# Optimization experiments

Hardware: AMD Instinct MI355X
Metric: run time of the kernel (lower is better)

Reference implementation:

```python
import jax, jax.numpy as jnp
import numpy as np

B, N, D, H, E, K = 8, 1024, 768, 12, 4, 9
PAD = (K - 1) // 2


def _ln(x, g, b, eps=1e-5):
    m = jnp.mean(x, -1, keepdims=True)
    v = jnp.var(x, -1, keepdims=True)
    return (x - m) * jax.lax.rsqrt(v + eps) * g + b


def setup_inputs() -> dict:
    key = jax.random.key(0)
    ks = jax.random.split(key, 12)
    w = lambda k, s: jax.random.normal(k, s, jnp.float32) * 0.02
    return {
        "x": jax.random.normal(ks[0], (B, N, D), jnp.float32),
        "ff1_ln_g": jnp.ones(D), "ff1_ln_b": jnp.zeros(D),
        "ff1_w1": w(ks[1], (D, E * D)), "ff1_b1": jnp.zeros(E * D),
        "ff1_w2": w(ks[2], (E * D, D)), "ff1_b2": jnp.zeros(D),
        "attn_ln_g": jnp.ones(D), "attn_ln_b": jnp.zeros(D),
        "qkv_w": w(ks[3], (D, 3 * D)), "qkv_b": jnp.zeros(3 * D),
        "proj_w": w(ks[4], (D, D)), "proj_b": jnp.zeros(D),
        "rel_table": w(ks[5], (2 * N - 1, H)),
        "conv_ln_g": jnp.ones(D), "conv_ln_b": jnp.zeros(D),
        "pwin_w": w(ks[6], (2 * D, D)), "pwin_b": jnp.zeros(2 * D),
        "dw_w": w(ks[7], (D, 1, K)), "dw_b": jnp.zeros(D),
        "bn_g": jnp.ones(D), "bn_b": jnp.zeros(D),
        "pwout_w": w(ks[8], (D, D)), "pwout_b": jnp.zeros(D),
        "ff2_ln_g": jnp.ones(D), "ff2_ln_b": jnp.zeros(D),
        "ff2_w1": w(ks[9], (D, E * D)), "ff2_b1": jnp.zeros(E * D),
        "ff2_w2": w(ks[10], (E * D, D)), "ff2_b2": jnp.zeros(D),
        "fin_ln_g": jnp.ones(D), "fin_ln_b": jnp.zeros(D),
    }


def _ffn(x, g, b, w1, b1, w2, b2):
    h = jax.nn.gelu(_ln(x, g, b) @ w1 + b1, approximate=False)
    return h @ w2 + b2


def _attn(x, qkv_w, qkv_b, proj_w, proj_b, rel_table):
    b_, n_, c = x.shape
    hd = c // H
    qkv = (x @ qkv_w + qkv_b).reshape(b_, n_, 3, H, hd).transpose(2, 0, 3, 1, 4)
    q, k, v = qkv[0], qkv[1], qkv[2]  # (B, H, N, hd)
    scores = jnp.einsum('bhqd,bhkd->bhqk', q, k) * (hd ** -0.5)
    coords = jnp.arange(n_)
    idx = coords[None, :] - coords[:, None] + N - 1  # (N, N) in [0, 2N-2]
    bias = rel_table[idx].transpose(2, 0, 1)  # (H, N, N)
    a = jax.nn.softmax(scores + bias[None], axis=-1)
    out = jnp.einsum('bhqk,bhkd->bhqd', a, v).transpose(0, 2, 1, 3).reshape(b_, n_, c)
    return out @ proj_w + proj_b


def _conv(x, g, b, pwin_w, pwin_b, dw_w, dw_b, bn_g, bn_b, pwout_w, pwout_b):
    y = _ln(x, g, b) @ pwin_w.T + pwin_b  # pointwise-in conv as matmul -> (B, N, 2D)
    u, gate = jnp.split(y, 2, axis=-1)
    y = (u * jax.nn.sigmoid(gate)).transpose(0, 2, 1)  # GLU over channels -> (B, D, N)
    y = jax.lax.conv_general_dilated(
        y, dw_w, (1,), [(PAD, PAD)], feature_group_count=D,
        dimension_numbers=('NCH', 'OIH', 'NCH')) + dw_b[None, :, None]
    m = jnp.mean(y, (0, 2), keepdims=True)  # BatchNorm1d, training-mode batch stats
    v = jnp.var(y, (0, 2), keepdims=True)
    y = (y - m) * jax.lax.rsqrt(v + 1e-5) * bn_g[None, :, None] + bn_b[None, :, None]
    y = y * jax.nn.sigmoid(y)  # SiLU
    y = jnp.einsum('bcn,oc->bno', y, pwout_w) + pwout_b  # pointwise-out, back to (B, N, D)
    return y


def reference(x, ff1_ln_g, ff1_ln_b, ff1_w1, ff1_b1, ff1_w2, ff1_b2,
              attn_ln_g, attn_ln_b, qkv_w, qkv_b, proj_w, proj_b, rel_table,
              conv_ln_g, conv_ln_b, pwin_w, pwin_b, dw_w, dw_b, bn_g, bn_b,
              pwout_w, pwout_b, ff2_ln_g, ff2_ln_b, ff2_w1, ff2_b1, ff2_w2, ff2_b2,
              fin_ln_g, fin_ln_b):
    x = x + 0.5 * _ffn(x, ff1_ln_g, ff1_ln_b, ff1_w1, ff1_b1, ff1_w2, ff1_b2)
    x = x + _attn(_ln(x, attn_ln_g, attn_ln_b), qkv_w, qkv_b, proj_w, proj_b, rel_table)
    x = x + _conv(x, conv_ln_g, conv_ln_b, pwin_w, pwin_b, dw_w, dw_b, bn_g, bn_b, pwout_w, pwout_b)
    x = x + 0.5 * _ffn(x, ff2_ln_g, ff2_ln_b, ff2_w1, ff2_b1, ff2_w2, ff2_b2)
    return _ln(x, fin_ln_g, fin_ln_b)
```

## Files before the change

### kernel.cpp

```cpp
#include <hip/hip_runtime.h>
#include <math.h>

#define Bb 8
#define Nn 1024
#define Dd 768
#define Hh 12
#define Mm 8192

typedef __attribute__((ext_vector_type(4))) float f32x4;
typedef __attribute__((ext_vector_type(8))) __bf16 bf16x8;

__device__ __forceinline__ float bf2f(unsigned short u) {
  union { unsigned int i; float f; } v; v.i = ((unsigned int)u) << 16; return v.f;
}
__device__ __forceinline__ unsigned short f2bf(float f) {
  union { float f; unsigned int i; } v; v.f = f;
  unsigned int u = v.i;
  return (unsigned short)((u + 0x7FFFu + ((u >> 16) & 1u)) >> 16);
}
__device__ __forceinline__ unsigned int pack2bf(float a, float b) {
  union { __bf16 h[2]; unsigned int u; } x;
  x.h[0] = (__bf16)a; x.h[1] = (__bf16)b; return x.u;
}

__device__ __forceinline__ void gload16(const void* g, void* l) {
  __builtin_amdgcn_global_load_lds(
      (const __attribute__((address_space(1))) unsigned int*)g,
      (__attribute__((address_space(3))) unsigned int*)l, 16, 0, 0);
}

__device__ __forceinline__ float gelu_f(float v) {
  const float z = fabsf(v) * 0.7071067811865475f;
  const float t = __builtin_amdgcn_rcpf(1.f + 0.3275911f * z);
  const float poly = t*(0.254829592f + t*(-0.284496736f + t*(1.421413741f +
                     t*(-1.453152027f + t*1.061405429f))));
  float er = 1.f - poly * __expf(-z * z);
  er = copysignf(er, v);
  return 0.5f * v * (1.f + er);
}

template<int EPI, int NT>
__global__ __launch_bounds__(256)
void gemm_bt(const unsigned short* __restrict__ A,
             const unsigned short* __restrict__ Bt,
             const float* __restrict__ bias,
             unsigned short* __restrict__ Cbf,
             float* __restrict__ Res,
             int M, int N, int K, float scale)
{
  __shared__ __align__(16) unsigned short Asm[128*32];
  __shared__ __align__(16) unsigned short Bsm[NT*32];
  const int tid = threadIdx.x;
  const int wv = tid >> 6, lane = tid & 63;
  const int lr = lane & 15, lg = lane >> 4;
  const int wr = wv >> 1, wc = wv & 1;
  constexpr int JN = NT / 32;

  const int gx = gridDim.x, gy = gridDim.y;
  const int nwg = gx * gy;
  const int lin = blockIdx.y * gx + blockIdx.x;
  const int q8 = nwg >> 3, r8 = nwg & 7;
  const int xcd = lin & 7, lidx = lin >> 3;
  const int wg = ((xcd < r8) ? xcd * (q8 + 1) : r8 * (q8 + 1) + (xcd - r8) * q8) + lidx;
  const int bx = wg % gx;
  const int by = wg / gx;

  const int n0 = bx * NT, m0 = by * 128;

  f32x4 acc[4][JN] = {};

  const int schk = (lane & 3) * 8;
  const unsigned short* Ag = A + (size_t)(m0 + wv*32 + (lane >> 2))*K + schk;
  unsigned short* Al = Asm + wv*1024;
  const unsigned short* Bg;
  unsigned short* Bl;
  if (NT == 128) { Bg = Bt + (size_t)(n0 + wv*32 + (lane >> 2))*K + schk; Bl = Bsm + wv*1024; }
  else           { Bg = Bt + (size_t)(n0 + wv*16 + (lane >> 2))*K + schk; Bl = Bsm + wv*512; }
  const size_t rstep = (size_t)16 * K;

  for (int kt = 0; kt < K; kt += 32) {
    gload16(Ag + kt,          Al);
    gload16(Ag + kt + rstep,  Al + 512);
    gload16(Bg + kt,          Bl);
    if (NT == 128) gload16(Bg + kt + rstep, Bl + 512);
    __syncthreads();
    bf16x8 af[4], bfr[JN];
#pragma unroll
    for (int i = 0; i < 4; i++) af[i]  = *(const bf16x8*)&Asm[(wr*64 + i*16 + lr)*32 + lg*8];
#pragma unroll
    for (int j = 0; j < JN; j++) bfr[j] = *(const bf16x8*)&Bsm[(wc*(NT/2) + j*16 + lr)*32 + lg*8];
#pragma unroll
    for (int i = 0; i < 4; i++)
#pragma unroll
      for (int j = 0; j < JN; j++)
        acc[i][j] = __builtin_amdgcn_mfma_f32_16x16x32_bf16(af[i], bfr[j], acc[i][j], 0, 0, 0);
    __syncthreads();
  }

#pragma unroll
  for (int i = 0; i < 4; i++) {
    const int rg = m0 + wr*64 + i*16 + lg*4;
    if (EPI == 3) {
#pragma unroll
      for (int j = 0; j < JN; j += 2) {
        const int cgu = n0 + wc*(NT/2) + j*16 + lr;
        const float bu = bias[cgu], bg = bias[cgu + 16];
        const int ocol = (n0 >> 1) + wc*(NT/4) + (j >> 1)*16 + lr;
#pragma unroll
        for (int e = 0; e < 4; e++) {
          float u  = acc[i][j][e]   + bu;
          float gt = acc[i][j+1][e] + bg;
          Cbf[(size_t)(rg + e) * (N >> 1) + ocol] = f2bf(u / (1.f + __expf(-gt)));
        }
      }
    } else {
#pragma unroll
      for (int j = 0; j < JN; j++) {
        const int cg = n0 + wc*(NT/2) + j*16 + lr;
        const float bv = bias[cg];
#pragma unroll
        for (int e = 0; e < 4; e++) {
          float v = acc[i][j][e] + bv;
          const size_t idx = (size_t)(rg + e) * N + cg;
          if (EPI == 1) {
            Cbf[idx] = f2bf(gelu_f(v));
          } else if (EPI == 0) {
            Cbf[idx] = f2bf(v);
          } else {
            Res[idx] += scale * v;
          }
        }
      }
    }
  }
}

template<bool OBF>
__global__ __launch_bounds__(256)
void ln_kernel(const float* x, const float* __restrict__ g,
               const float* __restrict__ b, void* out)
{
  const int row = blockIdx.x, tid = threadIdx.x;
  const float* xr = x + (size_t)row * Dd;
  float v0 = xr[tid], v1 = xr[tid+256], v2 = xr[tid+512];
  float s = v0+v1+v2, q = v0*v0+v1*v1+v2*v2;
  for (int off = 32; off; off >>= 1) { s += __shfl_down(s, off); q += __shfl_down(q, off); }
  __shared__ float ps[4], pq[4];
  if ((tid & 63) == 0) { ps[tid>>6] = s; pq[tid>>6] = q; }
  __syncthreads();
  s = ps[0]+ps[1]+ps[2]+ps[3]; q = pq[0]+pq[1]+pq[2]+pq[3];
  const float mean = s * (1.f/768.f);
  const float rstd = rsqrtf(q*(1.f/768.f) - mean*mean + 1e-5f);
  float y0 = (v0-mean)*rstd*g[tid]     + b[tid];
  float y1 = (v1-mean)*rstd*g[tid+256] + b[tid+256];
  float y2 = (v2-mean)*rstd*g[tid+512] + b[tid+512];
  if (OBF) {
    unsigned short* o = (unsigned short*)out + (size_t)row * Dd;
    o[tid] = f2bf(y0); o[tid+256] = f2bf(y1); o[tid+512] = f2bf(y2);
  } else {
    float* o = (float*)out + (size_t)row * Dd;
    o[tid] = y0; o[tid+256] = y1; o[tid+512] = y2;
  }
}

__global__ __launch_bounds__(256)
void transpose_w(const float* __restrict__ src, unsigned short* __restrict__ dst,
                 int K, int N)
{
  __shared__ float t[32][33];
  const int tx = threadIdx.x, ty = threadIdx.y;
  const int n0 = blockIdx.x * 32, k0 = blockIdx.y * 32;
#pragma unroll
  for (int i = 0; i < 4; i++) t[ty + i*8][tx] = src[(size_t)(k0 + ty + i*8)*N + n0 + tx];
  __syncthreads();
#pragma unroll
  for (int i = 0; i < 4; i++)
    dst[(size_t)(n0 + ty + i*8)*K + k0 + tx] = f2bf(t[tx][ty + i*8]);
}

__global__ __launch_bounds__(256)
void convert_bf(const float* __restrict__ src, unsigned short* __restrict__ dst, int n)
{
  for (int i = blockIdx.x*256 + threadIdx.x; i < n; i += gridDim.x*256)
    dst[i] = f2bf(src[i]);
}

__global__ __launch_bounds__(256)
void perm_pwin(const float* __restrict__ w, const float* __restrict__ b,
               unsigned short* __restrict__ wt, float* __restrict__ bperm)
{
  const int r = blockIdx.x;
  const int blk = r >> 7, g = (r >> 4) & 7, t = r & 15;
  const int orig = blk*64 + ((g >> 1) << 4) + t + ((g & 1) ? 768 : 0);
  const float* src = w + (size_t)orig * 768;
  unsigned short* dst = wt + (size_t)r * 768;
  const int tid = threadIdx.x;
  dst[tid] = f2bf(src[tid]); dst[tid+256] = f2bf(src[tid+256]); dst[tid+512] = f2bf(src[tid+512]);
  if (tid == 0) bperm[r] = b[orig];
}

__global__ __launch_bounds__(256)
void dw_tr(const float* __restrict__ src, float* __restrict__ dst)
{
  const int id = blockIdx.x*256 + threadIdx.x;
  if (id >= 9*768) return;
  const int k = id / 768, d = id % 768;
  dst[id] = src[d*9 + k];
}

__global__ __launch_bounds__(256)
void v_transpose(const unsigned short* __restrict__ big, unsigned short* __restrict__ vtr)
{
  __shared__ unsigned short t[64][72];
  const int bh = blockIdx.x;
  const int b = bh / Hh, h = bh % Hh;
  const int n0 = blockIdx.y * 64;
  const int tid = threadIdx.x;
  const int r = tid >> 2, cc = (tid & 3) * 16;
  const size_t gb = (size_t)(b*Nn + n0 + r)*2304 + 1536 + h*64 + cc;
  *(bf16x8*)&t[r][cc]     = *(const bf16x8*)(big + gb);
  *(bf16x8*)&t[r][cc + 8] = *(const bf16x8*)(big + gb + 8);
  __syncthreads();
  const int d = tid >> 2, nn = (tid & 3) * 16;
  bf16x8 o0, o1;
#pragma unroll
  for (int i = 0; i < 8; i++) o0[i] = *(const __bf16*)&t[nn + i][d];
#pragma unroll
  for (int i = 0; i < 8; i++) o1[i] = *(const __bf16*)&t[nn + 8 + i][d];
  unsigned short* dst = vtr + ((size_t)bh*64 + d)*Nn + n0 + nn;
  *(bf16x8*)dst = o0;
  *(bf16x8*)(dst + 8) = o1;
}

__global__ __launch_bounds__(256)
void attn_kernel(const unsigned short* __restrict__ qkv,
                 const unsigned short* __restrict__ vtr,
                 const float* __restrict__ rel,
                 unsigned short* __restrict__ out)
{
  const int bh = blockIdx.x; const int b = bh / Hh, h = bh % Hh;
  const int q0 = blockIdx.y * 64;
  const int tid = threadIdx.x, wv = tid >> 6, lane = tid & 63;
  const int lr = lane & 15, lg = lane >> 4;

  __shared__ __align__(16) unsigned short Kl[64*72];
  __shared__ __align__(16) unsigned short Vt[64*72 + 64];
  __shared__ __align__(16) unsigned short Pl[4*16*72];
  __shared__ float relh[2048];

  for (int i = tid; i < 2047; i += 256) relh[i] = rel[(size_t)i*Hh + h];

  const size_t qrow = (size_t)(b*Nn + q0 + wv*16 + lr);
  const bf16x8 qf0 = *(const bf16x8*)(qkv + qrow*2304 + h*64 + lg*8);
  const bf16x8 qf1 = *(const bf16x8*)(qkv + qrow*2304 + h*64 + 32 + lg*8);

  const int sd = tid >> 2;
  const int sc = (tid & 3) * 16;
  unsigned short* Pw = Pl + wv*16*72;

  f32x4 O[4] = {};
  float mrow = -1e30f, lsum = 0.f;
  const int qq = q0 + wv*16 + lr;

  __syncthreads();

  for (int kt = 0; kt < Nn; kt += 64) {
    {
      const size_t gk = (size_t)(b*Nn + kt + sd)*2304 + 768 + h*64 + sc;
      *(bf16x8*)&Kl[sd*72 + sc]     = *(const bf16x8*)(qkv + gk);
      *(bf16x8*)&Kl[sd*72 + sc + 8] = *(const bf16x8*)(qkv + gk + 8);
      const size_t gv = ((size_t)bh*64 + sd)*Nn + kt + sc;
      const int vb = sd*72 + (sd>>4)*16 + sc;
      *(bf16x8*)&Vt[vb]     = *(const bf16x8*)(vtr + gv);
      *(bf16x8*)&Vt[vb + 8] = *(const bf16x8*)(vtr + gv + 8);
    }
    __syncthreads();

    f32x4 s[4] = {};
#pragma unroll
    for (int kb = 0; kb < 4; kb++) {
      bf16x8 kfa = *(const bf16x8*)&Kl[(kb*16 + lr)*72 + lg*8];
      bf16x8 kfb = *(const bf16x8*)&Kl[(kb*16 + lr)*72 + 32 + lg*8];
      s[kb] = __builtin_amdgcn_mfma_f32_16x16x32_bf16(kfa, qf0, s[kb], 0, 0, 0);
      s[kb] = __builtin_amdgcn_mfma_f32_16x16x32_bf16(kfb, qf1, s[kb], 0, 0, 0);
    }

    const int bidx = kt - qq + (Nn - 1);
    float v[4][4]; float r = -1e30f;
#pragma unroll
    for (int kb = 0; kb < 4; kb++)
#pragma unroll
      for (int j = 0; j < 4; j++) {
        float t = s[kb][j]*0.125f + relh[bidx + kb*16 + lg*4 + j];
        v[kb][j] = t; r = fmaxf(r, t);
      }
    r = fmaxf(r, __shfl_xor(r, 16)); r = fmaxf(r, __shfl_xor(r, 32));

    if (!__all(r <= mrow + 8.f)) {
      const float mn = fmaxf(mrow, r);
      const float al = __expf(mrow - mn);
      mrow = mn;
      lsum *= al;
#pragma unroll
      for (int ni = 0; ni < 4; ni++) {
        O[ni][0]*=al; O[ni][1]*=al; O[ni][2]*=al; O[ni][3]*=al;
      }
    }

    float rs = 0.f;
    unsigned int pk[8];
#pragma unroll
    for (int kb = 0; kb < 4; kb++) {
      float p0 = __expf(v[kb][0]-mrow), p1 = __expf(v[kb][1]-mrow);
      float p2 = __expf(v[kb][2]-mrow), p3 = __expf(v[kb][3]-mrow);
      rs += (p0+p1) + (p2+p3);
      pk[kb*2]   = pack2bf(p0, p1);
      pk[kb*2+1] = pack2bf(p2, p3);
    }
    rs += __shfl_xor(rs, 16); rs += __shfl_xor(rs, 32);
    lsum += rs;

#pragma unroll
    for (int kb0 = 0; kb0 < 4; kb0++) {
      const int kb = (kb0 + lg) & 3;
      *(unsigned int*)&Pw[lr*72 + kb*16 + lg*4]     = pk[kb*2];
      *(unsigned int*)&Pw[lr*72 + kb*16 + lg*4 + 2] = pk[kb*2+1];
    }

    bf16x8 pf0 = *(const bf16x8*)&Pw[lr*72 + lg*8];
    bf16x8 pf1 = *(const bf16x8*)&Pw[lr*72 + 32 + lg*8];
#pragma unroll
    for (int dt = 0; dt < 4; dt++) {
      bf16x8 vf0 = *(const bf16x8*)&Vt[(dt*16 + lr)*72 + dt*16 + lg*8];
      bf16x8 vf1 = *(const bf16x8*)&Vt[(dt*16 + lr)*72 + dt*16 + 32 + lg*8];
      O[dt] = __builtin_amdgcn_mfma_f32_16x16x32_bf16(vf0, pf0, O[dt], 0, 0, 0);
      O[dt] = __builtin_amdgcn_mfma_f32_16x16x32_bf16(vf1, pf1, O[dt], 0, 0, 0);
    }
    __syncthreads();
  }

  const float rl = 1.f / lsum;
#pragma unroll
  for (int dt = 0; dt < 4; dt++) {
    ushort4 o4;
    o4.x = f2bf(O[dt][0]*rl); o4.y = f2bf(O[dt][1]*rl);
    o4.z = f2bf(O[dt][2]*rl); o4.w = f2bf(O[dt][3]*rl);
    *(ushort4*)(out + (size_t)(b*Nn + qq)*Dd + h*64 + dt*16 + lg*4) = o4;
  }
}

__global__ __launch_bounds__(256)
void dwconv(const unsigned short* __restrict__ glu, const float* __restrict__ dwwT,
            const float* __restrict__ dwb, unsigned short* __restrict__ z)
{
  const int id = blockIdx.x*256 + threadIdx.x;
  if (id >= Mm*96) return;
  const int row = id / 96, c8 = (id % 96) * 8;
  const int n = row % Nn;
  float acc[8] = {};
#pragma unroll
  for (int k = 0; k < 9; k++) {
    const int nn = n + k - 4;
    if (nn >= 0 && nn < Nn) {
      bf16x8 gv = *(const bf16x8*)&glu[(size_t)(row + k - 4)*768 + c8];
      const float4 w0 = *(const float4*)&dwwT[k*768 + c8];
      const float4 w1 = *(const float4*)&dwwT[k*768 + c8 + 4];
      acc[0] += w0.x*(float)gv[0]; acc[1] += w0.y*(float)gv[1];
      acc[2] += w0.z*(float)gv[2]; acc[3] += w0.w*(float)gv[3];
      acc[4] += w1.x*(float)gv[4]; acc[5] += w1.y*(float)gv[5];
      acc[6] += w1.z*(float)gv[6]; acc[7] += w1.w*(float)gv[7];
    }
  }
  bf16x8 o;
#pragma unroll
  for (int e = 0; e < 8; e++) o[e] = (__bf16)(acc[e] + dwb[c8+e]);
  *(bf16x8*)&z[(size_t)row*768 + c8] = o;
}

__global__ __launch_bounds__(256)
void bn_part(const unsigned short* __restrict__ z, float* __restrict__ psum,
             float* __restrict__ psq)
{
  const int blk = blockIdx.x, tid = threadIdx.x;
  float s[3] = {0,0,0}, q[3] = {0,0,0};
  for (int r = 0; r < 128; r++) {
    const unsigned short* row = z + (size_t)(blk*128 + r) * Dd;
#pragma unroll
    for (int i = 0; i < 3; i++) { float v = bf2f(row[tid + i*256]); s[i] += v; q[i] += v*v; }
  }
#pragma unroll
  for (int i = 0; i < 3; i++) {
    psum[(size_t)blk*Dd + tid + i*256] = s[i];
    psq [(size_t)blk*Dd + tid + i*256] = q[i];
  }
}

__global__ __launch_bounds__(256)
void bn_final(const float* __restrict__ psum, const float* __restrict__ psq,
              const float* __restrict__ g, const float* __restrict__ bb,
              float* __restrict__ scale, float* __restrict__ shift)
{
  const int c = blockIdx.x*256 + threadIdx.x;
  if (c >= Dd) return;
  float s = 0.f, q = 0.f;
  for (int i = 0; i < 64; i++) { s += psum[(size_t)i*Dd + c]; q += psq[(size_t)i*Dd + c]; }
  const float mean = s / (float)Mm;
  const float var  = q / (float)Mm - mean*mean;
  const float sc = g[c] * rsqrtf(var + 1e-5f);
  scale[c] = sc; shift[c] = bb[c] - mean*sc;
}

__global__ __launch_bounds__(256)
void bn_silu(const unsigned short* __restrict__ z, const float* __restrict__ scale,
             const float* __restrict__ shift, unsigned short* __restrict__ out)
{
  const int id = blockIdx.x*256 + threadIdx.x;
  if (id >= Mm * Dd) return;
  const int c = id % Dd;
  float v = bf2f(z[id]) * scale[c] + shift[c];
  v = v / (1.f + __expf(-v));
  out[id] = f2bf(v);
}

extern "C" void kernel_launch(void* const* d_in, const int* in_sizes, int n_in,
                              void* d_out, int out_size, void* d_ws, size_t ws_size,
                              hipStream_t stream)
{
  const float* x        = (const float*)d_in[0];
  const float* ff1_ln_g = (const float*)d_in[1];
  const float* ff1_ln_b = (const float*)d_in[2];
  const float* ff1_w1   = (const float*)d_in[3];
  const float* ff1_b1   = (const float*)d_in[4];
  const float* ff1_w2   = (const float*)d_in[5];
  const float* ff1_b2   = (const float*)d_in[6];
  const float* attn_ln_g= (const float*)d_in[7];
  const float* attn_ln_b= (const float*)d_in[8];
  const float* qkv_w    = (const float*)d_in[9];
  const float* qkv_b    = (const float*)d_in[10];
  const float* proj_w   = (const float*)d_in[11];
  const float* proj_b   = (const float*)d_in[12];
  const float* rel_tab  = (const float*)d_in[13];
  const float* conv_ln_g= (const float*)d_in[14];
  const float* conv_ln_b= (const float*)d_in[15];
  const float* pwin_w   = (const float*)d_in[16];
  const float* pwin_b   = (const float*)d_in[17];
  const float* dw_w     = (const float*)d_in[18];
  const float* dw_b     = (const float*)d_in[19];
  const float* bn_g     = (const float*)d_in[20];
  const float* bn_b     = (const float*)d_in[21];
  const float* pwout_w  = (const float*)d_in[22];
  const float* pwout_b  = (const float*)d_in[23];
  const float* ff2_ln_g = (const float*)d_in[24];
  const float* ff2_ln_b = (const float*)d_in[25];
  const float* ff2_w1   = (const float*)d_in[26];
  const float* ff2_b1   = (const float*)d_in[27];
  const float* ff2_w2   = (const float*)d_in[28];
  const float* ff2_b2   = (const float*)d_in[29];
  const float* fin_ln_g = (const float*)d_in[30];
  const float* fin_ln_b = (const float*)d_in[31];

  char* ws = (char*)d_ws;
  size_t off = 0;
  auto alloc = [&](size_t bytes) { char* p = ws + off; off += (bytes + 255) & ~(size_t)255; return p; };
  unsigned short* wt_ff1_1 = (unsigned short*)alloc((size_t)3072*768*2);
  unsigned short* wt_ff1_2 = (unsigned short*)alloc((size_t)768*3072*2);
  unsigned short* wt_qkv   = (unsigned short*)alloc((size_t)2304*768*2);
  unsigned short* wt_proj  = (unsigned short*)alloc((size_t)768*768*2);
  unsigned short* wt_pwin  = (unsigned short*)alloc((size_t)1536*768*2);
  unsigned short* wt_pwout = (unsigned short*)alloc((size_t)768*768*2);
  unsigned short* wt_ff2_1 = (unsigned short*)alloc((size_t)3072*768*2);
  unsigned short* wt_ff2_2 = (unsigned short*)alloc((size_t)768*3072*2);
  unsigned short* ybf      = (unsigned short*)alloc((size_t)Mm*768*2);
  unsigned short* big      = (unsigned short*)alloc((size_t)Mm*3072*2);
  unsigned short* abuf     = (unsigned short*)alloc((size_t)Mm*768*2);
  float* psum    = (float*)alloc((size_t)64*768*4);
  float* psq     = (float*)alloc((size_t)64*768*4);
  float* bnscale = (float*)alloc((size_t)768*4);
  float* bnshift = (float*)alloc((size_t)768*4);
  float* dwwT    = (float*)alloc((size_t)9*768*4);
  float* bperm   = (float*)alloc((size_t)1536*4);
  if (off > ws_size) return;

  unsigned short* vtr = ybf;

  float* xres = (float*)d_out;
  const dim3 tb(256);

  transpose_w<<<dim3(3072/32, 768/32), dim3(32,8), 0, stream>>>(ff1_w1, wt_ff1_1, 768, 3072);
  transpose_w<<<dim3(768/32, 3072/32), dim3(32,8), 0, stream>>>(ff1_w2, wt_ff1_2, 3072, 768);
  transpose_w<<<dim3(2304/32, 768/32), dim3(32,8), 0, stream>>>(qkv_w,  wt_qkv,  768, 2304);
  transpose_w<<<dim3(768/32, 768/32),  dim3(32,8), 0, stream>>>(proj_w, wt_proj, 768, 768);
  transpose_w<<<dim3(3072/32, 768/32), dim3(32,8), 0, stream>>>(ff2_w1, wt_ff2_1, 768, 3072);
  transpose_w<<<dim3(768/32, 3072/32), dim3(32,8), 0, stream>>>(ff2_w2, wt_ff2_2, 3072, 768);
  perm_pwin<<<1536, tb, 0, stream>>>(pwin_w, pwin_b, wt_pwin, bperm);
  convert_bf<<<2048, tb, 0, stream>>>(pwout_w, wt_pwout, 768*768);
  dw_tr<<<27, tb, 0, stream>>>(dw_w, dwwT);

  hipMemcpyAsync(d_out, (const void*)x, (size_t)Mm*Dd*4, hipMemcpyDeviceToDevice, stream);

  ln_kernel<true><<<Mm, tb, 0, stream>>>(xres, ff1_ln_g, ff1_ln_b, ybf);
  gemm_bt<1,128><<<dim3(3072/128, Mm/128), tb, 0, stream>>>(ybf, wt_ff1_1, ff1_b1, big, nullptr, Mm, 3072, 768, 0.f);
  gemm_bt<2,64><<<dim3(768/64, Mm/128), tb, 0, stream>>>(big, wt_ff1_2, ff1_b2, nullptr, xres, Mm, 768, 3072, 0.5f);

  ln_kernel<true><<<Mm, tb, 0, stream>>>(xres, attn_ln_g, attn_ln_b, ybf);
  gemm_bt<0,128><<<dim3(2304/128, Mm/128), tb, 0, stream>>>(ybf, wt_qkv, qkv_b, big, nullptr, Mm, 2304, 768, 0.f);
  v_transpose<<<dim3(Bb*Hh, Nn/64), tb, 0, stream>>>(big, vtr);
  attn_kernel<<<dim3(Bb*Hh, Nn/64), tb, 0, stream>>>(big, vtr, rel_tab, abuf);
  gemm_bt<2,64><<<dim3(768/64, Mm/128), tb, 0, stream>>>(abuf, wt_proj, proj_b, nullptr, xres, Mm, 768, 768, 1.0f);

  ln_kernel<true><<<Mm, tb, 0, stream>>>(xres, conv_ln_g, conv_ln_b, ybf);
  gemm_bt<3,128><<<dim3(1536/128, Mm/128), tb, 0, stream>>>(ybf, wt_pwin, bperm, abuf, nullptr, Mm, 1536, 768, 0.f);
  dwconv<<<(Mm*96)/256, tb, 0, stream>>>(abuf, dwwT, dw_b, ybf);
  bn_part<<<64, tb, 0, stream>>>(ybf, psum, psq);
  bn_final<<<3, tb, 0, stream>>>(psum, psq, bn_g, bn_b, bnscale, bnshift);
  bn_silu<<<(Mm*Dd)/256, tb, 0, stream>>>(ybf, bnscale, bnshift, abuf);
  gemm_bt<2,64><<<dim3(768/64, Mm/128), tb, 0, stream>>>(abuf, wt_pwout, pwout_b, nullptr, xres, Mm, 768, 768, 1.0f);

  ln_kernel<true><<<Mm, tb, 0, stream>>>(xres, ff2_ln_g, ff2_ln_b, ybf);
  gemm_bt<1,128><<<dim3(3072/128, Mm/128), tb, 0, stream>>>(ybf, wt_ff2_1, ff2_b1, big, nullptr, Mm, 3072, 768, 0.f);
  gemm_bt<2,64><<<dim3(768/64, Mm/128), tb, 0, stream>>>(big, wt_ff2_2, ff2_b2, nullptr, xres, Mm, 768, 3072, 0.5f);

  ln_kernel<false><<<Mm, tb, 0, stream>>>(xres, fin_ln_g, fin_ln_b, (void*)xres);
}
```

Before: 645.0 us.

## Use K=64 swizzled GEMM tiles, exp2 softmax, and fuse input copy into residual

The GEMM mainloop now stages 64-wide K slices with an XOR-swizzled LDS layout. This halves the barrier count per K and is meant to reduce LDS bank conflicts, at the cost of twice the shared memory per block. Attention folds the 1/sqrt(d) scale and log2(e) into Q and the relative-position table, so it can use the native exp2 and a matching rescale threshold. The initial device-to-device copy of x is removed: a new epilogue variant writes x + 0.5*FFN directly, and the first LayerNorm reads x.

```diff
diff --git a/kernel.cpp b/kernel.cpp
--- a/kernel.cpp
+++ b/kernel.cpp
@@ -46,10 +46,11 @@
              const float* __restrict__ bias,
              unsigned short* __restrict__ Cbf,
              float* __restrict__ Res,
+             const float* __restrict__ Xin,
              int M, int N, int K, float scale)
 {
-  __shared__ __align__(16) unsigned short Asm[128*32];
-  __shared__ __align__(16) unsigned short Bsm[NT*32];
+  __shared__ __align__(16) unsigned short Asm[128*64];
+  __shared__ __align__(16) unsigned short Bsm[NT*64];
   const int tid = threadIdx.x;
   const int wv = tid >> 6, lane = tid & 63;
   const int lr = lane & 15, lg = lane >> 4;
@@ -69,31 +70,48 @@
 
   f32x4 acc[4][JN] = {};
 
-  const int schk = (lane & 3) * 8;
-  const unsigned short* Ag = A + (size_t)(m0 + wv*32 + (lane >> 2))*K + schk;
-  unsigned short* Al = Asm + wv*1024;
-  const unsigned short* Bg;
-  unsigned short* Bl;
-  if (NT == 128) { Bg = Bt + (size_t)(n0 + wv*32 + (lane >> 2))*K + schk; Bl = Bsm + wv*1024; }
-  else           { Bg = Bt + (size_t)(n0 + wv*16 + (lane >> 2))*K + schk; Bl = Bsm + wv*512; }
-  const size_t rstep = (size_t)16 * K;
-
-  for (int kt = 0; kt < K; kt += 32) {
-    gload16(Ag + kt,          Al);
-    gload16(Ag + kt + rstep,  Al + 512);
-    gload16(Bg + kt,          Bl);
-    if (NT == 128) gload16(Bg + kt + rstep, Bl + 512);
+  const int srow8 = lane >> 3;
+  const int scol  = ((lane & 7) ^ srow8) * 8;
+  const unsigned short* Agp = A + (size_t)(m0 + wv*32 + srow8)*K + scol;
+  const unsigned short* Bgp = (NT == 128)
+      ? Bt + (size_t)(n0 + wv*32 + srow8)*K + scol
+      : Bt + (size_t)(n0 + wv*16 + srow8)*K + scol;
+  const int swr = (lr & 7) << 4;
+
+  for (int kt = 0; kt < K; kt += 64) {
+#pragma unroll
+    for (int k = 0; k < 4; k++)
+      gload16(Agp + (size_t)(k*8)*K + kt, Asm + (wv*32 + k*8)*64);
+    if (NT == 128) {
+#pragma unroll
+      for (int k = 0; k < 4; k++)
+        gload16(Bgp + (size_t)(k*8)*K + kt, Bsm + (wv*32 + k*8)*64);
+    } else {
+#pragma unroll
+      for (int k = 0; k < 2; k++)
+        gload16(Bgp + (size_t)(k*8)*K + kt, Bsm + (wv*16 + k*8)*64);
+    }
     __syncthreads();
-    bf16x8 af[4], bfr[JN];
-#pragma unroll
-    for (int i = 0; i < 4; i++) af[i]  = *(const bf16x8*)&Asm[(wr*64 + i*16 + lr)*32 + lg*8];
-#pragma unroll
-    for (int j = 0; j < JN; j++) bfr[j] = *(const bf16x8*)&Bsm[(wc*(NT/2) + j*16 + lr)*32 + lg*8];
+    bf16x8 af[4], af2[4], bfr[JN], bfr2[JN];
+#pragma unroll
+    for (int i = 0; i < 4; i++) {
+      const char* base = (const char*)Asm + (wr*64 + i*16 + lr)*128;
+      af[i]  = *(const bf16x8*)(base + ((lg*16)      ^ swr));
+      af2[i] = *(const bf16x8*)(base + ((lg*16 + 64) ^ swr));
+    }
+#pragma unroll
+    for (int j = 0; j < JN; j++) {
+      const char* base = (const char*)Bsm + (wc*(NT/2) + j*16 + lr)*128;
+      bfr[j]  = *(const bf16x8*)(base + ((lg*16)      ^ swr));
+      bfr2[j] = *(const bf16x8*)(base + ((lg*16 + 64) ^ swr));
+    }
 #pragma unroll
     for (int i = 0; i < 4; i++)
 #pragma unroll
-      for (int j = 0; j < JN; j++)
-        acc[i][j] = __builtin_amdgcn_mfma_f32_16x16x32_bf16(af[i], bfr[j], acc[i][j], 0, 0, 0);
+      for (int j = 0; j < JN; j++) {
+        acc[i][j] = __builtin_amdgcn_mfma_f32_16x16x32_bf16(af[i],  bfr[j],  acc[i][j], 0, 0, 0);
+        acc[i][j] = __builtin_amdgcn_mfma_f32_16x16x32_bf16(af2[i], bfr2[j], acc[i][j], 0, 0, 0);
+      }
     __syncthreads();
   }
 
@@ -126,8 +144,10 @@
             Cbf[idx] = f2bf(gelu_f(v));
           } else if (EPI == 0) {
             Cbf[idx] = f2bf(v);
+          } else if (EPI == 2) {
+            Res[idx] += scale * v;
           } else {
-            Res[idx] += scale * v;
+            Res[idx] = Xin[idx] + scale * v;
           }
         }
       }
@@ -248,11 +268,17 @@
   __shared__ __align__(16) unsigned short Pl[4*16*72];
   __shared__ float relh[2048];
 
-  for (int i = tid; i < 2047; i += 256) relh[i] = rel[(size_t)i*Hh + h];
+  for (int i = tid; i < 2047; i += 256) relh[i] = rel[(size_t)i*Hh + h] * 1.44269504f;
 
   const size_t qrow = (size_t)(b*Nn + q0 + wv*16 + lr);
-  const bf16x8 qf0 = *(const bf16x8*)(qkv + qrow*2304 + h*64 + lg*8);
-  const bf16x8 qf1 = *(const bf16x8*)(qkv + qrow*2304 + h*64 + 32 + lg*8);
+  const bf16x8 qraw0 = *(const bf16x8*)(qkv + qrow*2304 + h*64 + lg*8);
+  const bf16x8 qraw1 = *(const bf16x8*)(qkv + qrow*2304 + h*64 + 32 + lg*8);
+  bf16x8 qf0, qf1;
+#pragma unroll
+  for (int e = 0; e < 8; e++) {
+    qf0[e] = (__bf16)((float)qraw0[e] * 0.180336884f);
+    qf1[e] = (__bf16)((float)qraw1[e] * 0.180336884f);
+  }
 
   const int sd = tid >> 2;
   const int sc = (tid & 3) * 16;
@@ -291,14 +317,14 @@
     for (int kb = 0; kb < 4; kb++)
 #pragma unroll
       for (int j = 0; j < 4; j++) {
-        float t = s[kb][j]*0.125f + relh[bidx + kb*16 + lg*4 + j];
+        float t = s[kb][j] + relh[bidx + kb*16 + lg*4 + j];
         v[kb][j] = t; r = fmaxf(r, t);
       }
     r = fmaxf(r, __shfl_xor(r, 16)); r = fmaxf(r, __shfl_xor(r, 32));
 
-    if (!__all(r <= mrow + 8.f)) {
+    if (!__all(r <= mrow + 11.5f)) {
       const float mn = fmaxf(mrow, r);
-      const float al = __expf(mrow - mn);
+      const float al = __builtin_amdgcn_exp2f(mrow - mn);
       mrow = mn;
       lsum *= al;
 #pragma unroll
@@ -311,8 +337,8 @@
     unsigned int pk[8];
 #pragma unroll
     for (int kb = 0; kb < 4; kb++) {
-      float p0 = __expf(v[kb][0]-mrow), p1 = __expf(v[kb][1]-mrow);
-      float p2 = __expf(v[kb][2]-mrow), p3 = __expf(v[kb][3]-mrow);
+      float p0 = __builtin_amdgcn_exp2f(v[kb][0]-mrow), p1 = __builtin_amdgcn_exp2f(v[kb][1]-mrow);
+      float p2 = __builtin_amdgcn_exp2f(v[kb][2]-mrow), p3 = __builtin_amdgcn_exp2f(v[kb][3]-mrow);
       rs += (p0+p1) + (p2+p3);
       pk[kb*2]   = pack2bf(p0, p1);
       pk[kb*2+1] = pack2bf(p2, p3);
@@ -496,29 +522,27 @@
   convert_bf<<<2048, tb, 0, stream>>>(pwout_w, wt_pwout, 768*768);
   dw_tr<<<27, tb, 0, stream>>>(dw_w, dwwT);
 
-  hipMemcpyAsync(d_out, (const void*)x, (size_t)Mm*Dd*4, hipMemcpyDeviceToDevice, stream);
-
-  ln_kernel<true><<<Mm, tb, 0, stream>>>(xres, ff1_ln_g, ff1_ln_b, ybf);
-  gemm_bt<1,128><<<dim3(3072/128, Mm/128), tb, 0, stream>>>(ybf, wt_ff1_1, ff1_b1, big, nullptr, Mm, 3072, 768, 0.f);
-  gemm_bt<2,64><<<dim3(768/64, Mm/128), tb, 0, stream>>>(big, wt_ff1_2, ff1_b2, nullptr, xres, Mm, 768, 3072, 0.5f);
+  ln_kernel<true><<<Mm, tb, 0, stream>>>(x, ff1_ln_g, ff1_ln_b, ybf);
+  gemm_bt<1,128><<<dim3(3072/128, Mm/128), tb, 0, stream>>>(ybf, wt_ff1_1, ff1_b1, big, nullptr, nullptr, Mm, 3072, 768, 0.f);
+  gemm_bt<4,64><<<dim3(768/64, Mm/128), tb, 0, stream>>>(big, wt_ff1_2, ff1_b2, nullptr, xres, x, Mm, 768, 3072, 0.5f);
 
   ln_kernel<true><<<Mm, tb, 0, stream>>>(xres, attn_ln_g, attn_ln_b, ybf);
-  gemm_bt<0,128><<<dim3(2304/128, Mm/128), tb, 0, stream>>>(ybf, wt_qkv, qkv_b, big, nullptr, Mm, 2304, 768, 0.f);
+  gemm_bt<0,128><<<dim3(2304/128, Mm/128), tb, 0, stream>>>(ybf, wt_qkv, qkv_b, big, nullptr, nullptr, Mm, 2304, 768, 0.f);
   v_transpose<<<dim3(Bb*Hh, Nn/64), tb, 0, stream>>>(big, vtr);
   attn_kernel<<<dim3(Bb*Hh, Nn/64), tb, 0, stream>>>(big, vtr, rel_tab, abuf);
-  gemm_bt<2,64><<<dim3(768/64, Mm/128), tb, 0, stream>>>(abuf, wt_proj, proj_b, nullptr, xres, Mm, 768, 768, 1.0f);
+  gemm_bt<2,64><<<dim3(768/64, Mm/128), tb, 0, stream>>>(abuf, wt_proj, proj_b, nullptr, xres, nullptr, Mm, 768, 768, 1.0f);
 
   ln_kernel<true><<<Mm, tb, 0, stream>>>(xres, conv_ln_g, conv_ln_b, ybf);
-  gemm_bt<3,128><<<dim3(1536/128, Mm/128), tb, 0, stream>>>(ybf, wt_pwin, bperm, abuf, nullptr, Mm, 1536, 768, 0.f);
+  gemm_bt<3,128><<<dim3(1536/128, Mm/128), tb, 0, stream>>>(ybf, wt_pwin, bperm, abuf, nullptr, nullptr, Mm, 1536, 768, 0.f);
   dwconv<<<(Mm*96)/256, tb, 0, stream>>>(abuf, dwwT, dw_b, ybf);
   bn_part<<<64, tb, 0, stream>>>(ybf, psum, psq);
   bn_final<<<3, tb, 0, stream>>>(psum, psq, bn_g, bn_b, bnscale, bnshift);
   bn_silu<<<(Mm*Dd)/256, tb, 0, stream>>>(ybf, bnscale, bnshift, abuf);
-  gemm_bt<2,64><<<dim3(768/64, Mm/128), tb, 0, stream>>>(abuf, wt_pwout, pwout_b, nullptr, xres, Mm, 768, 768, 1.0f);
+  gemm_bt<2,64><<<dim3(768/64, Mm/128), tb, 0, stream>>>(abuf, wt_pwout, pwout_b, nullptr, xres, nullptr, Mm, 768, 768, 1.0f);
 
   ln_kernel<true><<<Mm, tb, 0, stream>>>(xres, ff2_ln_g, ff2_ln_b, ybf);
-  gemm_bt<1,128><<<dim3(3072/128, Mm/128), tb, 0, stream>>>(ybf, wt_ff2_1, ff2_b1, big, nullptr, Mm, 3072, 768, 0.f);
-  gemm_bt<2,64><<<dim3(768/64, Mm/128), tb, 0, stream>>>(big, wt_ff2_2, ff2_b2, nullptr, xres, Mm, 768, 3072, 0.5f);
+  gemm_bt<1,128><<<dim3(3072/128, Mm/128), tb, 0, stream>>>(ybf, wt_ff2_1, ff2_b1, big, nullptr, nullptr, Mm, 3072, 768, 0.f);
+  gemm_bt<2,64><<<dim3(768/64, Mm/128), tb, 0, stream>>>(big, wt_ff2_2, ff2_b2, nullptr, xres, nullptr, Mm, 768, 3072, 0.5f);
 
   ln_kernel<false><<<Mm, tb, 0, stream>>>(xres, fin_ln_g, fin_ln_b, (void*)xres);
 }
```

Measured after the change: 565.7 us. -12.3%, faster.
